# Optimization experiments

Hardware: AMD Instinct MI355X
Metric: run time of the kernel (lower is better)

Reference implementation:

```python
import math
import jax, jax.numpy as jnp
import numpy as np

HEAD_DIM = 128
NUM_HEADS = 16
NUM_KV_HEADS = 4
CAUSAL = True


def rotate_half(x):
    x1 = x[..., : x.shape[-1] // 2]
    x2 = x[..., x.shape[-1] // 2 :]
    return jnp.concatenate([-x2, x1], axis=-1)


def setup_inputs() -> dict:
    key = jax.random.key(0)
    k1, k2, k3, k4, k5 = jax.random.split(key, 5)
    B, S, H = 2, 2048, 2048
    total_heads = NUM_HEADS + 2 * NUM_KV_HEADS  # 24
    hidden_states = jax.random.normal(k1, (B, S, H), dtype=jnp.float32)
    cos = jax.random.normal(k2, (S, HEAD_DIM), dtype=jnp.float32)
    sin = jax.random.normal(k3, (S, HEAD_DIM), dtype=jnp.float32)
    # eqx.nn.Linear weight layout: [out_features, in_features], y = W @ x
    w_qkv = jax.random.normal(k4, (total_heads * HEAD_DIM, H), dtype=jnp.float32) / math.sqrt(H)
    w_o = jax.random.normal(k5, (H, NUM_HEADS * HEAD_DIM), dtype=jnp.float32) / math.sqrt(NUM_HEADS * HEAD_DIM)
    return {"hidden_states": hidden_states, "cos": cos, "sin": sin, "w_qkv": w_qkv, "w_o": w_o}


def reference(hidden_states, cos, sin, w_qkv, w_o):
    B, S, _ = hidden_states.shape
    # fused QKV projection: [B,S,total_heads,head_dim]
    qkv = jnp.einsum("bsh,oh->bso", hidden_states, w_qkv).reshape(B, S, -1, HEAD_DIM)
    q = qkv[:, :, :NUM_HEADS]
    k = qkv[:, :, NUM_HEADS : NUM_HEADS + NUM_KV_HEADS]
    v = qkv[:, :, NUM_HEADS + NUM_KV_HEADS :]
    # RoPE: cos/sin [S,head_dim] -> broadcast [S,1,head_dim] over heads
    c = cos[..., None, :]
    s_ = sin[..., None, :]
    q = q * c + rotate_half(q) * s_
    k = k * c + rotate_half(k) * s_
    # GQA: repeat K/V across query-head groups
    rep = NUM_HEADS // NUM_KV_HEADS
    k = jnp.repeat(k, rep, axis=2)
    v = jnp.repeat(v, rep, axis=2)
    scale = 1.0 / math.sqrt(HEAD_DIM)
    scores = jnp.einsum("bshd,bthd->bhst", q, k) * scale  # [B,H,S,S]
    if CAUSAL:
        mask = jnp.tril(jnp.ones((S, S), dtype=bool))[None, None]
        scores = jnp.where(mask, scores, jnp.float32(-1e10))
    attn = jax.nn.softmax(scores, axis=-1)
    out = jnp.einsum("bhst,bthd->bshd", attn, v).reshape(B, S, -1)
    return jnp.einsum("bsd,od->bso", out, w_o)
```

## Files before the change

### kernel.cpp

```cpp
#include <hip/hip_runtime.h>
#include <hip/hip_bf16.h>
#include <stdint.h>

typedef __hip_bfloat16 bf16;
typedef __attribute__((ext_vector_type(8))) __bf16 bf16x8;
typedef __attribute__((ext_vector_type(4))) float f32x4;
typedef __attribute__((ext_vector_type(16))) float f32x16;
typedef __attribute__((ext_vector_type(4))) unsigned int u32x4;

#define QSCALE_LOG2E (0.08838834764831845f * 1.4426950408889634f)

__device__ __forceinline__ float fast_exp2(float x) {
#if __has_builtin(__builtin_amdgcn_exp2f)
  return __builtin_amdgcn_exp2f(x);
#else
  return exp2f(x);
#endif
}

__device__ __forceinline__ void gload_lds16(const void* g, void* l) {
  __builtin_amdgcn_global_load_lds(
      (__attribute__((address_space(1))) void*)(uintptr_t)g,
      (__attribute__((address_space(3))) void*)(uint32_t)(uintptr_t)l,
      16, 0, 0);
}

__global__ void cast3(const float* __restrict__ h, const float* __restrict__ wq,
                      const float* __restrict__ wo, bf16* __restrict__ oh,
                      bf16* __restrict__ owq, bf16* __restrict__ owo) {
  const int total = 4718592;
  const int stride = gridDim.x * blockDim.x;
  for (int c = blockIdx.x * blockDim.x + threadIdx.x; c < total; c += stride) {
    const float* src;
    bf16* dst;
    int i;
    if (c < 2097152) { src = h; dst = oh; i = c; }
    else if (c < 3670016) { src = wq; dst = owq; i = c - 2097152; }
    else { src = wo; dst = owo; i = c - 3670016; }
    float4 v = reinterpret_cast<const float4*>(src)[i];
    bf16 tmp[4];
    tmp[0] = __float2bfloat16(v.x);
    tmp[1] = __float2bfloat16(v.y);
    tmp[2] = __float2bfloat16(v.z);
    tmp[3] = __float2bfloat16(v.w);
    reinterpret_cast<uint2*>(dst)[i] = *reinterpret_cast<uint2*>(tmp);
  }
}

__device__ __forceinline__ void store_c(float v, bf16* p) { *p = __float2bfloat16(v); }
__device__ __forceinline__ void store_c(float v, float* p) { *p = v; }

__device__ __forceinline__ bf16x8 rd_swz(const bf16* base, int row, int ks, int hi) {
  const int byte = row * 128 + ((ks * 64 + hi * 16) ^ ((row & 7) << 4));
  return *reinterpret_cast<const bf16x8*>((const char*)base + byte);
}

__device__ __forceinline__ void stage_part(const bf16* __restrict__ g, int K,
                                           int kt, bf16* ldsBase, int part,
                                           int tid) {
  const int ga = part * 512 + tid;
  const int r = ga >> 3;
  const int gl = ga & 7;
  const int col = kt * 64 + ((gl ^ (r & 7)) << 3);
  gload_lds16(g + (size_t)r * K + col, (char*)ldsBase + ga * 16);
}

#define DS_A(QR)                                                              \
  _Pragma("unroll") for (int m = 0; m < 4; ++m)                               \
  _Pragma("unroll") for (int ks = 0; ks < 2; ++ks)                            \
      af[m][ks] = rd_swz(Acur, wm * 128 + (QR) * 64 + m * 16 + lr, ks, hi);

#define DS_B0()                                                               \
  _Pragma("unroll") for (int n = 0; n < NQ0; ++n)                             \
  _Pragma("unroll") for (int ks = 0; ks < 2; ++ks)                            \
      bf0[n][ks] = rd_swz(Bcur, wn * WN + n * 16 + lr, ks, hi);

#define DS_B1()                                                               \
  _Pragma("unroll") for (int n = 0; n < NQ1; ++n)                             \
  _Pragma("unroll") for (int ks = 0; ks < 2; ++ks)                            \
      bf1[n][ks] = rd_swz(Bcur, wn * WN + (NQ0 + n) * 16 + lr, ks, hi);

#define MFMA_Q0(QR)                                                           \
  __builtin_amdgcn_s_setprio(1);                                             \
  _Pragma("unroll") for (int ks = 0; ks < 2; ++ks)                            \
  _Pragma("unroll") for (int m = 0; m < 4; ++m)                               \
  _Pragma("unroll") for (int n = 0; n < NQ0; ++n)                             \
      acc[(QR) * 4 + m][n] = __builtin_amdgcn_mfma_f32_16x16x32_bf16(         \
          af[m][ks], bf0[n][ks], acc[(QR) * 4 + m][n], 0, 0, 0);              \
  __builtin_amdgcn_s_setprio(0);

#define MFMA_Q1(QR)                                                           \
  __builtin_amdgcn_s_setprio(1);                                             \
  _Pragma("unroll") for (int ks = 0; ks < 2; ++ks)                            \
  _Pragma("unroll") for (int m = 0; m < 4; ++m)                               \
  _Pragma("unroll") for (int n = 0; n < NQ1; ++n)                             \
      acc[(QR) * 4 + m][NQ0 + n] = __builtin_amdgcn_mfma_f32_16x16x32_bf16(   \
          af[m][ks], bf1[n][ks], acc[(QR) * 4 + m][NQ0 + n], 0, 0, 0);        \
  __builtin_amdgcn_s_setprio(0);

#define PHASE_SYNC_PRE()                                \
  __builtin_amdgcn_s_barrier();                         \
  asm volatile("s_waitcnt lgkmcnt(0)" ::: "memory");    \
  __builtin_amdgcn_sched_barrier(0);

#define PHASE_END() __builtin_amdgcn_s_barrier();

#define VMCNT_LB()                                                            \
  if constexpr (LB == 2) asm volatile("s_waitcnt vmcnt(2)" ::: "memory");     \
  else if constexpr (LB == 3) asm volatile("s_waitcnt vmcnt(3)" ::: "memory");\
  else asm volatile("s_waitcnt vmcnt(4)" ::: "memory");

template <int BN, typename OutT>
__global__ __launch_bounds__(512, 2) void gemm256(const bf16* __restrict__ A,
                                                  const bf16* __restrict__ B,
                                                  OutT* __restrict__ C,
                                                  int M, int N, int K, int NBX) {
  constexpr int NFRAG = BN / 64;
  constexpr int NQ0 = (NFRAG + 1) / 2;
  constexpr int NQ1 = NFRAG - NQ0;
  constexpr int WN = BN / 4;
  constexpr int LB = BN / 64;
  constexpr int LB0 = (LB + 1) / 2;
  constexpr int LB1 = LB - LB0;

  extern __shared__ bf16 sm[];
  bf16* A0 = sm;
  bf16* A1 = sm + 16384;
  bf16* B0 = sm + 32768;
  bf16* B1 = B0 + BN * 64;

  const int tid = threadIdx.x;
  const int lane = tid & 63;
  const int w = tid >> 6;
  const int wm = w >> 2;
  const int wn = w & 3;
  const int lr = lane & 15;
  const int hi = lane >> 4;

  const int nwg = gridDim.x;
  const int cpx = nwg >> 3;
  const int bid = blockIdx.x;
  const int wg = (bid & 7) * cpx + (bid >> 3);
  const int bx = wg % NBX;
  const int by = wg / NBX;
  const int row0 = by * 256;
  const int col0 = bx * BN;

  const bf16* Ag = A + (size_t)row0 * K;
  const bf16* Bg = B + (size_t)col0 * K;

#pragma unroll
  for (int p = 0; p < 4; ++p) stage_part(Ag, K, 0, A0, p, tid);
#pragma unroll
  for (int p = 0; p < LB; ++p) stage_part(Bg, K, 0, B0, p, tid);
#pragma unroll
  for (int p = 0; p < LB; ++p) stage_part(Bg, K, 1, B1, p, tid);
  VMCNT_LB();
  __builtin_amdgcn_s_barrier();

  f32x4 acc[8][NFRAG] = {};
  bf16x8 af[4][2], bf0[NQ0][2], bf1[NQ1 ? NQ1 : 1][2];

  const int iters = K >> 7;
  for (int i = 0; i < iters; ++i) {
    const bool g2 = (i + 1 < iters);
    const int t1 = 2 * i + 1, t2 = 2 * i + 2, t3 = 2 * i + 3;
    {
      const bf16* Acur = A0;
      const bf16* Bcur = B0;
      DS_A(0); DS_B0();
      stage_part(Ag, K, t1, A1, 0, tid);
      stage_part(Ag, K, t1, A1, 1, tid);
      PHASE_SYNC_PRE(); MFMA_Q0(0); PHASE_END();
      DS_B1();
      stage_part(Ag, K, t1, A1, 2, tid);
      stage_part(Ag, K, t1, A1, 3, tid);
      PHASE_SYNC_PRE(); MFMA_Q1(0); PHASE_END();
      DS_A(1);
      if (g2) {
#pragma unroll
        for (int p = 0; p < LB0; ++p) stage_part(Bg, K, t2, B0, p, tid);
      }
      PHASE_SYNC_PRE(); MFMA_Q0(1); PHASE_END();
      if (g2) {
#pragma unroll
        for (int p = 0; p < LB1; ++p) stage_part(Bg, K, t2, B0, LB0 + p, tid);
        VMCNT_LB();
      } else {
        asm volatile("s_waitcnt vmcnt(0)" ::: "memory");
      }
      PHASE_SYNC_PRE(); MFMA_Q1(1); PHASE_END();
    }
    {
      const bf16* Acur = A1;
      const bf16* Bcur = B1;
      DS_A(0); DS_B0();
      if (g2) {
        stage_part(Ag, K, t2, A0, 0, tid);
        stage_part(Ag, K, t2, A0, 1, tid);
      }
      PHASE_SYNC_PRE(); MFMA_Q0(0); PHASE_END();
      DS_B1();
      if (g2) {
        stage_part(Ag, K, t2, A0, 2, tid);
        stage_part(Ag, K, t2, A0, 3, tid);
      }
      PHASE_SYNC_PRE(); MFMA_Q1(0); PHASE_END();
      DS_A(1);
      if (g2) {
#pragma unroll
        for (int p = 0; p < LB0; ++p) stage_part(Bg, K, t3, B1, p, tid);
      }
      PHASE_SYNC_PRE(); MFMA_Q0(1); PHASE_END();
      if (g2) {
#pragma unroll
        for (int p = 0; p < LB1; ++p) stage_part(Bg, K, t3, B1, LB0 + p, tid);
        VMCNT_LB();
      } else {
        asm volatile("s_waitcnt vmcnt(0)" ::: "memory");
      }
      PHASE_SYNC_PRE(); MFMA_Q1(1); PHASE_END();
    }
  }

#pragma unroll
  for (int mi = 0; mi < 8; ++mi)
#pragma unroll
    for (int ni = 0; ni < NFRAG; ++ni)
#pragma unroll
      for (int j = 0; j < 4; ++j) {
        const int r = row0 + wm * 128 + mi * 16 + hi * 4 + j;
        const int cc = col0 + wn * WN + ni * 16 + lr;
        store_c(acc[mi][ni][j], &C[(size_t)r * N + cc]);
      }
}

__global__ void rope_scatter(const bf16* __restrict__ qkv,
                             const float* __restrict__ cs,
                             const float* __restrict__ sn,
                             bf16* __restrict__ Q, bf16* __restrict__ Kd) {
  const int tok = blockIdx.x;
  const int b = tok >> 11;
  const int s = tok & 2047;
  const bf16* row = qkv + (size_t)tok * 3072;
  for (int idx = threadIdx.x; idx < 1280; idx += blockDim.x) {
    const int head = idx >> 6;
    const int j = idx & 63;
    float x1 = __bfloat162float(row[head * 128 + j]);
    float x2 = __bfloat162float(row[head * 128 + j + 64]);
    const float c1 = cs[s * 128 + j];
    const float c2 = cs[s * 128 + j + 64];
    const float s1 = sn[s * 128 + j];
    const float s2 = sn[s * 128 + j + 64];
    float y1 = x1 * c1 - x2 * s1;
    float y2 = x2 * c2 + x1 * s2;
    bf16* dst;
    if (head < 16) {
      y1 *= QSCALE_LOG2E;
      y2 *= QSCALE_LOG2E;
      dst = Q + ((size_t)(b * 16 + head) * 2048 + s) * 128;
    } else {
      dst = Kd + ((size_t)(b * 4 + head - 16) * 2048 + s) * 128;
    }
    dst[j] = __float2bfloat16(y1);
    dst[j + 64] = __float2bfloat16(y2);
  }
}

__global__ __launch_bounds__(256) void vtrans(const bf16* __restrict__ qkv,
                                              bf16* __restrict__ Vt) {
  __shared__ bf16 tile[64 * 136];
  const int bid = blockIdx.x;
  const int stile = bid & 31;
  const int hv = (bid >> 5) & 3;
  const int b = bid >> 7;
  const int tid = threadIdx.x;
  const int tok0 = stile * 64;
  const bf16* src = qkv + (size_t)(b * 2048 + tok0) * 3072 + 2560 + hv * 128;
#pragma unroll
  for (int i = 0; i < 4; ++i) {
    const int c = tid + i * 256;
    const int r = c >> 4;
    const int off = (c & 15) * 8;
    uint4 d = *reinterpret_cast<const uint4*>(src + (size_t)r * 3072 + off);
    *reinterpret_cast<uint4*>(&tile[r * 136 + off]) = d;
  }
  __syncthreads();
  bf16* dst = Vt + ((size_t)(b * 4 + hv) * 128) * 2048 + tok0;
#pragma unroll
  for (int i = 0; i < 4; ++i) {
    const int o = tid + i * 256;
    const int d = o >> 3;
    const int s0 = (o & 7) * 8;
    bf16 vals[8];
#pragma unroll
    for (int j = 0; j < 8; ++j) vals[j] = tile[(s0 + j) * 136 + d];
    *reinterpret_cast<uint4*>(dst + (size_t)d * 2048 + s0) =
        *reinterpret_cast<const uint4*>(vals);
  }
}

__device__ __forceinline__ void stage_k(const bf16* __restrict__ Kb, int k0,
                                        bf16* dst, int w, int lane) {
#pragma unroll
  for (int i = 0; i < 4; ++i) {
    const int L16 = i * 256 + w * 64 + lane;
    const int row = L16 >> 4;
    const int colb = (L16 & 15) * 16;
    const int src = colb ^ ((row & 7) << 4);
    gload_lds16(Kb + (size_t)(k0 + row) * 128 + (src >> 1),
                (char*)dst + (i * 256 + w * 64) * 16);
  }
}

__device__ __forceinline__ void stage_v(const bf16* __restrict__ Vtb, int k0,
                                        bf16* dst, int w, int lane) {
#pragma unroll
  for (int i = 0; i < 4; ++i) {
    const int L16 = i * 256 + w * 64 + lane;
    const int row = L16 >> 3;
    const int colb = (L16 & 7) * 16;
    const int src = colb ^ ((row & 7) << 4);
    gload_lds16(Vtb + (size_t)row * 2048 + k0 + (src >> 1),
                (char*)dst + (i * 256 + w * 64) * 16);
  }
}

__device__ __forceinline__ bf16x8 lds_read_swz(const bf16* base, int row,
                                               int colElem, int rowBytes) {
  const int byte = row * rowBytes + (((colElem * 2) ^ ((row & 7) << 4)));
  return *reinterpret_cast<const bf16x8*>((const char*)base + byte);
}

__global__ __launch_bounds__(256, 2) void attn_fwd(const bf16* __restrict__ Qg,
                                                   const bf16* __restrict__ Kg,
                                                   const bf16* __restrict__ Vtg,
                                                   bf16* __restrict__ Og) {
  __shared__ bf16 Ks[2][64 * 128];
  __shared__ bf16 Vs[2][128 * 64];

  const int tid = threadIdx.x;
  const int lane = tid & 63;
  const int w = tid >> 6;
  const int bid = blockIdx.x;
  int qt, bh;
  if (bid < 256) { qt = bid & 15; bh = bid >> 4; }
  else           { qt = 15 - (bid & 15); bh = 16 + ((bid - 256) >> 4); }
  const int b = bh >> 4;
  const int h = bh & 15;
  const int kvh = h >> 2;
  const int q31 = lane & 31;
  const int hw = lane >> 5;

  const bf16* Qb = Qg + ((size_t)(b * 16 + h) * 2048) * 128;
  const bf16* Kb = Kg + ((size_t)(b * 4 + kvh) * 2048) * 128;
  const bf16* Vtb = Vtg + ((size_t)(b * 4 + kvh) * 128) * 2048;

  const int qw = qt * 128 + w * 32;

  bf16x8 qf[8];
#pragma unroll
  for (int db = 0; db < 8; ++db)
    qf[db] = *reinterpret_cast<const bf16x8*>(Qb + (size_t)(qw + q31) * 128 +
                                              db * 16 + hw * 8);

  f32x16 acc[4] = {};
  float mrow = -1e30f;
  float lsum = 0.f;

  const int nt = 2 * qt + 2;

  stage_k(Kb, 0, &Ks[0][0], w, lane);
  stage_v(Vtb, 0, &Vs[0][0], w, lane);

  for (int t = 0; t < nt; ++t) {
    const int cur = t & 1;
    if (t + 1 < nt) {
      stage_k(Kb, (t + 1) * 64, &Ks[cur ^ 1][0], w, lane);
      stage_v(Vtb, (t + 1) * 64, &Vs[cur ^ 1][0], w, lane);
      asm volatile("s_waitcnt vmcnt(8)" ::: "memory");
    } else {
      asm volatile("s_waitcnt vmcnt(0)" ::: "memory");
    }
    __builtin_amdgcn_s_barrier();
    __builtin_amdgcn_sched_barrier(0);

    const int k0 = t * 64;
    const bool active = (k0 <= qw + 31);
    if (active) {
      const bf16* Kt = &Ks[cur][0];
      const bf16* Vtl = &Vs[cur][0];

      bf16x8 va[8];
#pragma unroll
      for (int i = 0; i < 8; ++i) {
        const int kb16 = i >> 2, db = i & 3;
        va[i] = lds_read_swz(Vtl, db * 32 + q31, kb16 * 16 + hw * 8, 128);
      }

      f32x16 sacc[2] = {};
      __builtin_amdgcn_s_setprio(1);
#pragma unroll
      for (int kb = 0; kb < 2; ++kb)
#pragma unroll
        for (int db = 0; db < 8; ++db) {
          bf16x8 kf = lds_read_swz(Kt, kb * 32 + q31, db * 16 + hw * 8, 256);
          sacc[kb] = __builtin_amdgcn_mfma_f32_32x32x16_bf16(kf, qf[db],
                                                             sacc[kb], 0, 0, 0);
        }
      __builtin_amdgcn_s_setprio(0);

      bf16x8 vb[8];
#pragma unroll
      for (int i = 0; i < 8; ++i) {
        const int kb16 = 2 + (i >> 2), db = i & 3;
        vb[i] = lds_read_swz(Vtl, db * 32 + q31, kb16 * 16 + hw * 8, 128);
      }

      float p[2][16];
#pragma unroll
      for (int kb = 0; kb < 2; ++kb)
#pragma unroll
        for (int r = 0; r < 16; ++r) p[kb][r] = sacc[kb][r];

      if (k0 + 63 > qw) {
        const int qg = qw + q31;
#pragma unroll
        for (int kb = 0; kb < 2; ++kb)
#pragma unroll
          for (int r = 0; r < 16; ++r) {
            const int k = k0 + kb * 32 + (r & 3) + 8 * (r >> 2) + 4 * hw;
            if (k > qg) p[kb][r] = -1e30f;
          }
      }

      float mt = p[0][0];
#pragma unroll
      for (int r = 1; r < 16; ++r) mt = fmaxf(mt, p[0][r]);
#pragma unroll
      for (int r = 0; r < 16; ++r) mt = fmaxf(mt, p[1][r]);
      mt = fmaxf(mt, __shfl_xor(mt, 32));

      if (__any(mt > mrow + 11.5f)) {
        const float mnew = fmaxf(mrow, mt);
        const float alpha = fast_exp2(mrow - mnew);
        mrow = mnew;
        lsum *= alpha;
        float areg[16];
#pragma unroll
        for (int r = 0; r < 16; ++r) {
          const int qloc = (r & 3) + 8 * (r >> 2) + 4 * hw;
          areg[r] = __shfl(alpha, qloc + (lane & 32));
        }
#pragma unroll
        for (int db = 0; db < 4; ++db)
#pragma unroll
          for (int r = 0; r < 16; ++r) acc[db][r] *= areg[r];
      }

      float rs = 0.f;
#pragma unroll
      for (int kb = 0; kb < 2; ++kb)
#pragma unroll
        for (int r = 0; r < 16; ++r) {
          const float pe = fast_exp2(p[kb][r] - mrow);
          p[kb][r] = pe;
          rs += pe;
        }
      rs += __shfl_xor(rs, 32);
      lsum += rs;

      unsigned int pk[2][8];
#pragma unroll
      for (int kb = 0; kb < 2; ++kb)
#pragma unroll
        for (int i = 0; i < 8; ++i)
          asm("v_cvt_pk_bf16_f32 %0, %1, %2"
              : "=v"(pk[kb][i])
              : "v"(p[kb][2 * i]), "v"(p[kb][2 * i + 1]));

#pragma unroll
      for (int kb16 = 0; kb16 < 4; ++kb16) {
        const int kb = kb16 >> 1;
        const int j0 = (kb16 & 1) * 4;
        unsigned int a0 = pk[kb][j0 + 0], b0 = pk[kb][j0 + 2];
        unsigned int a1 = pk[kb][j0 + 1], b1 = pk[kb][j0 + 3];
        asm volatile("v_permlane32_swap_b32 %0, %1" : "+v"(a0), "+v"(b0));
        asm volatile("v_permlane32_swap_b32 %0, %1" : "+v"(a1), "+v"(b1));
        u32x4 afu;
        afu.x = a0; afu.y = a1; afu.z = b0; afu.w = b1;
        bf16x8 pa;
        __builtin_memcpy(&pa, &afu, 16);
        __builtin_amdgcn_s_setprio(1);
#pragma unroll
        for (int db = 0; db < 4; ++db) {
          const bf16x8 vf = (kb16 < 2) ? va[kb16 * 4 + db] : vb[(kb16 - 2) * 4 + db];
          acc[db] = __builtin_amdgcn_mfma_f32_32x32x16_bf16(pa, vf,
                                                            acc[db], 0, 0, 0);
        }
        __builtin_amdgcn_s_setprio(0);
      }
    }

    __builtin_amdgcn_sched_barrier(0);
    __builtin_amdgcn_s_barrier();
  }

  const float inv = 1.0f / lsum;
  float invq[16];
#pragma unroll
  for (int r = 0; r < 16; ++r) {
    const int qloc = (r & 3) + 8 * (r >> 2) + 4 * hw;
    invq[r] = __shfl(inv, qloc + (lane & 32));
  }
#pragma unroll
  for (int db = 0; db < 4; ++db)
#pragma unroll
    for (int r = 0; r < 16; ++r) {
      const int qg = qw + (r & 3) + 8 * (r >> 2) + 4 * hw;
      const int dg = db * 32 + q31;
      Og[((size_t)(b * 2048 + qg)) * 2048 + h * 128 + dg] =
          __float2bfloat16(acc[db][r] * invq[r]);
    }
}

extern "C" void kernel_launch(void* const* d_in, const int* in_sizes, int n_in,
                              void* d_out, int out_size, void* d_ws,
                              size_t ws_size, hipStream_t stream) {
  const float* hidden = (const float*)d_in[0];
  const float* cs = (const float*)d_in[1];
  const float* sn = (const float*)d_in[2];
  const float* wqkv = (const float*)d_in[3];
  const float* wo = (const float*)d_in[4];
  float* out = (float*)d_out;

  bf16* p = (bf16*)d_ws;
  bf16* hid_b = p;   p += 8388608;
  bf16* wqkv_b = p;  p += 6291456;
  bf16* wo_b = p;    p += 4194304;
  bf16* qkv = p;     p += 12582912;
  bf16* Qs = p;      p += 8388608;
  bf16* Ksc = p;     p += 2097152;
  bf16* Vt = p;      p += 2097152;

  (void)hipFuncSetAttribute((const void*)gemm256<192, bf16>,
                            hipFuncAttributeMaxDynamicSharedMemorySize, 131072);
  (void)hipFuncSetAttribute((const void*)gemm256<128, float>,
                            hipFuncAttributeMaxDynamicSharedMemorySize, 131072);

  cast3<<<2048, 256, 0, stream>>>(hidden, wqkv, wo, hid_b, wqkv_b, wo_b);

  gemm256<192, bf16><<<256, 512, 114688, stream>>>(hid_b, wqkv_b, qkv,
                                                   4096, 3072, 2048, 16);
  rope_scatter<<<4096, 256, 0, stream>>>(qkv, cs, sn, Qs, Ksc);
  vtrans<<<256, 256, 0, stream>>>(qkv, Vt);

  bf16* aout = hid_b;
  attn_fwd<<<512, 256, 0, stream>>>(Qs, Ksc, Vt, aout);

  gemm256<128, float><<<256, 512, 98304, stream>>>(aout, wo_b, out,
                                                   4096, 2048, 2048, 16);
}
```

Before: 174.8 us.

## Give each attention wave two 32-row query tiles, halving block size

The attention kernel now runs 2 waves per block (128 threads) instead of 4, and each wave handles 64 query rows as two 32-row sub-tiles. Each K and V fragment read from LDS is reused across both sub-tiles, which halves LDS read traffic per MFMA. The staging loops are rewritten for 128 threads, with 8 loads each and a matching vmcnt wait. In exchange, per-wave register use roughly doubles (two accumulator sets, Q fragments and score tiles), and there are fewer waves per block to hide latency. The causal skip is also coarser, at 64-row granularity.

```diff
diff --git a/kernel.cpp b/kernel.cpp
--- a/kernel.cpp
+++ b/kernel.cpp
@@ -300,29 +300,29 @@
   }
 }
 
-__device__ __forceinline__ void stage_k(const bf16* __restrict__ Kb, int k0,
-                                        bf16* dst, int w, int lane) {
-#pragma unroll
-  for (int i = 0; i < 4; ++i) {
-    const int L16 = i * 256 + w * 64 + lane;
-    const int row = L16 >> 4;
-    const int colb = (L16 & 15) * 16;
+__device__ __forceinline__ void stage_k2(const bf16* __restrict__ Kb, int k0,
+                                         bf16* dst, int tid) {
+#pragma unroll
+  for (int i = 0; i < 8; ++i) {
+    const int ga = i * 128 + tid;
+    const int row = ga >> 4;
+    const int colb = (ga & 15) << 4;
     const int src = colb ^ ((row & 7) << 4);
     gload_lds16(Kb + (size_t)(k0 + row) * 128 + (src >> 1),
-                (char*)dst + (i * 256 + w * 64) * 16);
-  }
-}
-
-__device__ __forceinline__ void stage_v(const bf16* __restrict__ Vtb, int k0,
-                                        bf16* dst, int w, int lane) {
-#pragma unroll
-  for (int i = 0; i < 4; ++i) {
-    const int L16 = i * 256 + w * 64 + lane;
-    const int row = L16 >> 3;
-    const int colb = (L16 & 7) * 16;
+                (char*)dst + ga * 16);
+  }
+}
+
+__device__ __forceinline__ void stage_v2(const bf16* __restrict__ Vtb, int k0,
+                                         bf16* dst, int tid) {
+#pragma unroll
+  for (int i = 0; i < 8; ++i) {
+    const int ga = i * 128 + tid;
+    const int row = ga >> 3;
+    const int colb = (ga & 7) << 4;
     const int src = colb ^ ((row & 7) << 4);
     gload_lds16(Vtb + (size_t)row * 2048 + k0 + (src >> 1),
-                (char*)dst + (i * 256 + w * 64) * 16);
+                (char*)dst + ga * 16);
   }
 }
 
@@ -332,7 +332,7 @@
   return *reinterpret_cast<const bf16x8*>((const char*)base + byte);
 }
 
-__global__ __launch_bounds__(256, 2) void attn_fwd(const bf16* __restrict__ Qg,
+__global__ __launch_bounds__(128, 1) void attn_fwd(const bf16* __restrict__ Qg,
                                                    const bf16* __restrict__ Kg,
                                                    const bf16* __restrict__ Vtg,
                                                    bf16* __restrict__ Og) {
@@ -356,29 +356,31 @@
   const bf16* Kb = Kg + ((size_t)(b * 4 + kvh) * 2048) * 128;
   const bf16* Vtb = Vtg + ((size_t)(b * 4 + kvh) * 128) * 2048;
 
-  const int qw = qt * 128 + w * 32;
-
-  bf16x8 qf[8];
-#pragma unroll
-  for (int db = 0; db < 8; ++db)
-    qf[db] = *reinterpret_cast<const bf16x8*>(Qb + (size_t)(qw + q31) * 128 +
-                                              db * 16 + hw * 8);
-
-  f32x16 acc[4] = {};
-  float mrow = -1e30f;
-  float lsum = 0.f;
+  const int qw = qt * 128 + w * 64;
+
+  bf16x8 qf[2][8];
+#pragma unroll
+  for (int qt2 = 0; qt2 < 2; ++qt2)
+#pragma unroll
+    for (int db = 0; db < 8; ++db)
+      qf[qt2][db] = *reinterpret_cast<const bf16x8*>(
+          Qb + (size_t)(qw + qt2 * 32 + q31) * 128 + db * 16 + hw * 8);
+
+  f32x16 acc[2][4] = {};
+  float mrow[2] = {-1e30f, -1e30f};
+  float lsum[2] = {0.f, 0.f};
 
   const int nt = 2 * qt + 2;
 
-  stage_k(Kb, 0, &Ks[0][0], w, lane);
-  stage_v(Vtb, 0, &Vs[0][0], w, lane);
+  stage_k2(Kb, 0, &Ks[0][0], tid);
+  stage_v2(Vtb, 0, &Vs[0][0], tid);
 
   for (int t = 0; t < nt; ++t) {
     const int cur = t & 1;
     if (t + 1 < nt) {
-      stage_k(Kb, (t + 1) * 64, &Ks[cur ^ 1][0], w, lane);
-      stage_v(Vtb, (t + 1) * 64, &Vs[cur ^ 1][0], w, lane);
-      asm volatile("s_waitcnt vmcnt(8)" ::: "memory");
+      stage_k2(Kb, (t + 1) * 64, &Ks[cur ^ 1][0], tid);
+      stage_v2(Vtb, (t + 1) * 64, &Vs[cur ^ 1][0], tid);
+      asm volatile("s_waitcnt vmcnt(16)" ::: "memory");
     } else {
       asm volatile("s_waitcnt vmcnt(0)" ::: "memory");
     }
@@ -386,117 +388,126 @@
     __builtin_amdgcn_sched_barrier(0);
 
     const int k0 = t * 64;
-    const bool active = (k0 <= qw + 31);
-    if (active) {
+    if (k0 <= qw + 63) {
       const bf16* Kt = &Ks[cur][0];
       const bf16* Vtl = &Vs[cur][0];
 
-      bf16x8 va[8];
-#pragma unroll
-      for (int i = 0; i < 8; ++i) {
-        const int kb16 = i >> 2, db = i & 3;
-        va[i] = lds_read_swz(Vtl, db * 32 + q31, kb16 * 16 + hw * 8, 128);
-      }
-
-      f32x16 sacc[2] = {};
-      __builtin_amdgcn_s_setprio(1);
-#pragma unroll
-      for (int kb = 0; kb < 2; ++kb)
-#pragma unroll
-        for (int db = 0; db < 8; ++db) {
-          bf16x8 kf = lds_read_swz(Kt, kb * 32 + q31, db * 16 + hw * 8, 256);
-          sacc[kb] = __builtin_amdgcn_mfma_f32_32x32x16_bf16(kf, qf[db],
-                                                             sacc[kb], 0, 0, 0);
+      f32x16 sacc[2][2] = {};
+#pragma unroll
+      for (int kb = 0; kb < 2; ++kb) {
+        bf16x8 kf[8];
+#pragma unroll
+        for (int db = 0; db < 8; ++db)
+          kf[db] = lds_read_swz(Kt, kb * 32 + q31, db * 16 + hw * 8, 256);
+        __builtin_amdgcn_s_setprio(1);
+#pragma unroll
+        for (int qt2 = 0; qt2 < 2; ++qt2)
+#pragma unroll
+          for (int db = 0; db < 8; ++db)
+            sacc[qt2][kb] = __builtin_amdgcn_mfma_f32_32x32x16_bf16(
+                kf[db], qf[qt2][db], sacc[qt2][kb], 0, 0, 0);
+        __builtin_amdgcn_s_setprio(0);
+      }
+
+      float p[2][2][16];
+#pragma unroll
+      for (int qt2 = 0; qt2 < 2; ++qt2)
+#pragma unroll
+        for (int kb = 0; kb < 2; ++kb)
+#pragma unroll
+          for (int r = 0; r < 16; ++r) p[qt2][kb][r] = sacc[qt2][kb][r];
+
+#pragma unroll
+      for (int qt2 = 0; qt2 < 2; ++qt2) {
+        if (k0 + 63 > qw + qt2 * 32) {
+          const int qg = qw + qt2 * 32 + q31;
+#pragma unroll
+          for (int kb = 0; kb < 2; ++kb)
+#pragma unroll
+            for (int r = 0; r < 16; ++r) {
+              const int k = k0 + kb * 32 + (r & 3) + 8 * (r >> 2) + 4 * hw;
+              if (k > qg) p[qt2][kb][r] = -1e30f;
+            }
         }
-      __builtin_amdgcn_s_setprio(0);
-
-      bf16x8 vb[8];
-#pragma unroll
-      for (int i = 0; i < 8; ++i) {
-        const int kb16 = 2 + (i >> 2), db = i & 3;
-        vb[i] = lds_read_swz(Vtl, db * 32 + q31, kb16 * 16 + hw * 8, 128);
-      }
-
-      float p[2][16];
-#pragma unroll
-      for (int kb = 0; kb < 2; ++kb)
-#pragma unroll
-        for (int r = 0; r < 16; ++r) p[kb][r] = sacc[kb][r];
-
-      if (k0 + 63 > qw) {
-        const int qg = qw + q31;
+      }
+
+      float mt[2];
+#pragma unroll
+      for (int qt2 = 0; qt2 < 2; ++qt2) {
+        float m = p[qt2][0][0];
+#pragma unroll
+        for (int r = 1; r < 16; ++r) m = fmaxf(m, p[qt2][0][r]);
+#pragma unroll
+        for (int r = 0; r < 16; ++r) m = fmaxf(m, p[qt2][1][r]);
+        mt[qt2] = fmaxf(m, __shfl_xor(m, 32));
+      }
+
+      if (__any((mt[0] > mrow[0] + 11.5f) || (mt[1] > mrow[1] + 11.5f))) {
+#pragma unroll
+        for (int qt2 = 0; qt2 < 2; ++qt2) {
+          const float mnew = fmaxf(mrow[qt2], mt[qt2]);
+          const float alpha = fast_exp2(mrow[qt2] - mnew);
+          mrow[qt2] = mnew;
+          lsum[qt2] *= alpha;
+          float areg[16];
+#pragma unroll
+          for (int r = 0; r < 16; ++r) {
+            const int qloc = (r & 3) + 8 * (r >> 2) + 4 * hw;
+            areg[r] = __shfl(alpha, qloc + (lane & 32));
+          }
+#pragma unroll
+          for (int db = 0; db < 4; ++db)
+#pragma unroll
+            for (int r = 0; r < 16; ++r) acc[qt2][db][r] *= areg[r];
+        }
+      }
+
+      unsigned int pk[2][2][8];
+#pragma unroll
+      for (int qt2 = 0; qt2 < 2; ++qt2) {
+        float rs = 0.f;
 #pragma unroll
         for (int kb = 0; kb < 2; ++kb)
 #pragma unroll
           for (int r = 0; r < 16; ++r) {
-            const int k = k0 + kb * 32 + (r & 3) + 8 * (r >> 2) + 4 * hw;
-            if (k > qg) p[kb][r] = -1e30f;
+            const float pe = fast_exp2(p[qt2][kb][r] - mrow[qt2]);
+            p[qt2][kb][r] = pe;
+            rs += pe;
           }
-      }
-
-      float mt = p[0][0];
-#pragma unroll
-      for (int r = 1; r < 16; ++r) mt = fmaxf(mt, p[0][r]);
-#pragma unroll
-      for (int r = 0; r < 16; ++r) mt = fmaxf(mt, p[1][r]);
-      mt = fmaxf(mt, __shfl_xor(mt, 32));
-
-      if (__any(mt > mrow + 11.5f)) {
-        const float mnew = fmaxf(mrow, mt);
-        const float alpha = fast_exp2(mrow - mnew);
-        mrow = mnew;
-        lsum *= alpha;
-        float areg[16];
-#pragma unroll
-        for (int r = 0; r < 16; ++r) {
-          const int qloc = (r & 3) + 8 * (r >> 2) + 4 * hw;
-          areg[r] = __shfl(alpha, qloc + (lane & 32));
-        }
+        rs += __shfl_xor(rs, 32);
+        lsum[qt2] += rs;
+#pragma unroll
+        for (int kb = 0; kb < 2; ++kb)
+#pragma unroll
+          for (int i = 0; i < 8; ++i)
+            asm("v_cvt_pk_bf16_f32 %0, %1, %2"
+                : "=v"(pk[qt2][kb][i])
+                : "v"(p[qt2][kb][2 * i]), "v"(p[qt2][kb][2 * i + 1]));
+      }
+
+#pragma unroll
+      for (int kb16 = 0; kb16 < 4; ++kb16) {
+        bf16x8 vf[4];
 #pragma unroll
         for (int db = 0; db < 4; ++db)
-#pragma unroll
-          for (int r = 0; r < 16; ++r) acc[db][r] *= areg[r];
-      }
-
-      float rs = 0.f;
-#pragma unroll
-      for (int kb = 0; kb < 2; ++kb)
-#pragma unroll
-        for (int r = 0; r < 16; ++r) {
-          const float pe = fast_exp2(p[kb][r] - mrow);
-          p[kb][r] = pe;
-          rs += pe;
-        }
-      rs += __shfl_xor(rs, 32);
-      lsum += rs;
-
-      unsigned int pk[2][8];
-#pragma unroll
-      for (int kb = 0; kb < 2; ++kb)
-#pragma unroll
-        for (int i = 0; i < 8; ++i)
-          asm("v_cvt_pk_bf16_f32 %0, %1, %2"
-              : "=v"(pk[kb][i])
-              : "v"(p[kb][2 * i]), "v"(p[kb][2 * i + 1]));
-
-#pragma unroll
-      for (int kb16 = 0; kb16 < 4; ++kb16) {
-        const int kb = kb16 >> 1;
-        const int j0 = (kb16 & 1) * 4;
-        unsigned int a0 = pk[kb][j0 + 0], b0 = pk[kb][j0 + 2];
-        unsigned int a1 = pk[kb][j0 + 1], b1 = pk[kb][j0 + 3];
-        asm volatile("v_permlane32_swap_b32 %0, %1" : "+v"(a0), "+v"(b0));
-        asm volatile("v_permlane32_swap_b32 %0, %1" : "+v"(a1), "+v"(b1));
-        u32x4 afu;
-        afu.x = a0; afu.y = a1; afu.z = b0; afu.w = b1;
-        bf16x8 pa;
-        __builtin_memcpy(&pa, &afu, 16);
+          vf[db] = lds_read_swz(Vtl, db * 32 + q31, kb16 * 16 + hw * 8, 128);
         __builtin_amdgcn_s_setprio(1);
 #pragma unroll
-        for (int db = 0; db < 4; ++db) {
-          const bf16x8 vf = (kb16 < 2) ? va[kb16 * 4 + db] : vb[(kb16 - 2) * 4 + db];
-          acc[db] = __builtin_amdgcn_mfma_f32_32x32x16_bf16(pa, vf,
-                                                            acc[db], 0, 0, 0);
+        for (int qt2 = 0; qt2 < 2; ++qt2) {
+          const int kb = kb16 >> 1;
+          const int j0 = (kb16 & 1) * 4;
+          unsigned int a0 = pk[qt2][kb][j0 + 0], b0 = pk[qt2][kb][j0 + 2];
+          unsigned int a1 = pk[qt2][kb][j0 + 1], b1 = pk[qt2][kb][j0 + 3];
+          asm volatile("v_permlane32_swap_b32 %0, %1" : "+v"(a0), "+v"(b0));
+          asm volatile("v_permlane32_swap_b32 %0, %1" : "+v"(a1), "+v"(b1));
+          u32x4 afu;
+          afu.x = a0; afu.y = a1; afu.z = b0; afu.w = b1;
+          bf16x8 pa;
+          __builtin_memcpy(&pa, &afu, 16);
+#pragma unroll
+          for (int db = 0; db < 4; ++db)
+            acc[qt2][db] = __builtin_amdgcn_mfma_f32_32x32x16_bf16(
+                pa, vf[db], acc[qt2][db], 0, 0, 0);
         }
         __builtin_amdgcn_s_setprio(0);
       }
@@ -506,22 +517,25 @@
     __builtin_amdgcn_s_barrier();
   }
 
-  const float inv = 1.0f / lsum;
-  float invq[16];
-#pragma unroll
-  for (int r = 0; r < 16; ++r) {
-    const int qloc = (r & 3) + 8 * (r >> 2) + 4 * hw;
-    invq[r] = __shfl(inv, qloc + (lane & 32));
-  }
-#pragma unroll
-  for (int db = 0; db < 4; ++db)
+#pragma unroll
+  for (int qt2 = 0; qt2 < 2; ++qt2) {
+    const float inv = 1.0f / lsum[qt2];
+    float invq[16];
 #pragma unroll
     for (int r = 0; r < 16; ++r) {
-      const int qg = qw + (r & 3) + 8 * (r >> 2) + 4 * hw;
-      const int dg = db * 32 + q31;
-      Og[((size_t)(b * 2048 + qg)) * 2048 + h * 128 + dg] =
-          __float2bfloat16(acc[db][r] * invq[r]);
+      const int qloc = (r & 3) + 8 * (r >> 2) + 4 * hw;
+      invq[r] = __shfl(inv, qloc + (lane & 32));
     }
+#pragma unroll
+    for (int db = 0; db < 4; ++db)
+#pragma unroll
+      for (int r = 0; r < 16; ++r) {
+        const int qg = qw + qt2 * 32 + (r & 3) + 8 * (r >> 2) + 4 * hw;
+        const int dg = db * 32 + q31;
+        Og[((size_t)(b * 2048 + qg)) * 2048 + h * 128 + dg] =
+            __float2bfloat16(acc[qt2][db][r] * invq[r]);
+      }
+  }
 }
 
 extern "C" void kernel_launch(void* const* d_in, const int* in_sizes, int n_in,
@@ -556,7 +570,7 @@
   vtrans<<<256, 256, 0, stream>>>(qkv, Vt);
 
   bf16* aout = hid_b;
-  attn_fwd<<<512, 256, 0, stream>>>(Qs, Ksc, Vt, aout);
+  attn_fwd<<<512, 128, 0, stream>>>(Qs, Ksc, Vt, aout);
 
   gemm256<128, float><<<256, 512, 98304, stream>>>(aout, wo_b, out,
                                                    4096, 2048, 2048, 16);
```

Result: slower. 238.2 us (+36.3%).

## Triple-buffer A in GEMM with 64-wide K steps; load V fragments on demand

Applied to the files above, without the earlier changes.

The GEMM main loop changes from paired ping-pong steps over 128-wide K to a single 64-wide K-step loop. A gets three LDS buffers and is prefetched two tiles ahead, while B stays double-buffered and is prefetched one tile ahead. The goal is to hide more global-load latency, at the cost of more LDS per block (the dynamic shared size is raised to match). In attention, V fragments are now read from LDS right before each PV MFMA instead of being preloaded into registers, and the s_setprio hints are removed, which trades register pressure for LDS-read latency on the critical path.

```diff
diff --git a/kernel.cpp b/kernel.cpp
--- a/kernel.cpp
+++ b/kernel.cpp
@@ -105,11 +105,6 @@
 
 #define PHASE_END() __builtin_amdgcn_s_barrier();
 
-#define VMCNT_LB()                                                            \
-  if constexpr (LB == 2) asm volatile("s_waitcnt vmcnt(2)" ::: "memory");     \
-  else if constexpr (LB == 3) asm volatile("s_waitcnt vmcnt(3)" ::: "memory");\
-  else asm volatile("s_waitcnt vmcnt(4)" ::: "memory");
-
 template <int BN, typename OutT>
 __global__ __launch_bounds__(512, 2) void gemm256(const bf16* __restrict__ A,
                                                   const bf16* __restrict__ B,
@@ -120,14 +115,12 @@
   constexpr int NQ1 = NFRAG - NQ0;
   constexpr int WN = BN / 4;
   constexpr int LB = BN / 64;
-  constexpr int LB0 = (LB + 1) / 2;
-  constexpr int LB1 = LB - LB0;
+  constexpr int LB1 = (LB > 2) ? 2 : LB;
+  constexpr int LB2 = LB - LB1;
 
   extern __shared__ bf16 sm[];
-  bf16* A0 = sm;
-  bf16* A1 = sm + 16384;
-  bf16* B0 = sm + 32768;
-  bf16* B1 = B0 + BN * 64;
+  bf16* Ab = sm;
+  bf16* Bb = sm + 3 * 16384;
 
   const int tid = threadIdx.x;
   const int lane = tid & 63;
@@ -150,77 +143,52 @@
   const bf16* Bg = B + (size_t)col0 * K;
 
 #pragma unroll
-  for (int p = 0; p < 4; ++p) stage_part(Ag, K, 0, A0, p, tid);
-#pragma unroll
-  for (int p = 0; p < LB; ++p) stage_part(Bg, K, 0, B0, p, tid);
-#pragma unroll
-  for (int p = 0; p < LB; ++p) stage_part(Bg, K, 1, B1, p, tid);
-  VMCNT_LB();
+  for (int p = 0; p < 4; ++p) stage_part(Ag, K, 0, Ab, p, tid);
+#pragma unroll
+  for (int p = 0; p < 4; ++p) stage_part(Ag, K, 1, Ab + 16384, p, tid);
+#pragma unroll
+  for (int p = 0; p < LB; ++p) stage_part(Bg, K, 0, Bb, p, tid);
+  asm volatile("s_waitcnt vmcnt(0)" ::: "memory");
   __builtin_amdgcn_s_barrier();
 
   f32x4 acc[8][NFRAG] = {};
   bf16x8 af[4][2], bf0[NQ0][2], bf1[NQ1 ? NQ1 : 1][2];
 
-  const int iters = K >> 7;
-  for (int i = 0; i < iters; ++i) {
-    const bool g2 = (i + 1 < iters);
-    const int t1 = 2 * i + 1, t2 = 2 * i + 2, t3 = 2 * i + 3;
-    {
-      const bf16* Acur = A0;
-      const bf16* Bcur = B0;
-      DS_A(0); DS_B0();
-      stage_part(Ag, K, t1, A1, 0, tid);
-      stage_part(Ag, K, t1, A1, 1, tid);
-      PHASE_SYNC_PRE(); MFMA_Q0(0); PHASE_END();
-      DS_B1();
-      stage_part(Ag, K, t1, A1, 2, tid);
-      stage_part(Ag, K, t1, A1, 3, tid);
-      PHASE_SYNC_PRE(); MFMA_Q1(0); PHASE_END();
-      DS_A(1);
-      if (g2) {
-#pragma unroll
-        for (int p = 0; p < LB0; ++p) stage_part(Bg, K, t2, B0, p, tid);
-      }
-      PHASE_SYNC_PRE(); MFMA_Q0(1); PHASE_END();
-      if (g2) {
-#pragma unroll
-        for (int p = 0; p < LB1; ++p) stage_part(Bg, K, t2, B0, LB0 + p, tid);
-        VMCNT_LB();
-      } else {
-        asm volatile("s_waitcnt vmcnt(0)" ::: "memory");
-      }
-      PHASE_SYNC_PRE(); MFMA_Q1(1); PHASE_END();
-    }
-    {
-      const bf16* Acur = A1;
-      const bf16* Bcur = B1;
-      DS_A(0); DS_B0();
-      if (g2) {
-        stage_part(Ag, K, t2, A0, 0, tid);
-        stage_part(Ag, K, t2, A0, 1, tid);
-      }
-      PHASE_SYNC_PRE(); MFMA_Q0(0); PHASE_END();
-      DS_B1();
-      if (g2) {
-        stage_part(Ag, K, t2, A0, 2, tid);
-        stage_part(Ag, K, t2, A0, 3, tid);
-      }
-      PHASE_SYNC_PRE(); MFMA_Q1(0); PHASE_END();
-      DS_A(1);
-      if (g2) {
-#pragma unroll
-        for (int p = 0; p < LB0; ++p) stage_part(Bg, K, t3, B1, p, tid);
-      }
-      PHASE_SYNC_PRE(); MFMA_Q0(1); PHASE_END();
-      if (g2) {
-#pragma unroll
-        for (int p = 0; p < LB1; ++p) stage_part(Bg, K, t3, B1, LB0 + p, tid);
-        VMCNT_LB();
-      } else {
-        asm volatile("s_waitcnt vmcnt(0)" ::: "memory");
-      }
-      PHASE_SYNC_PRE(); MFMA_Q1(1); PHASE_END();
-    }
+  const int ntile = K >> 6;
+  for (int t = 0; t < ntile; ++t) {
+    const bf16* Acur = Ab + (t % 3) * 16384;
+    const bf16* Bcur = Bb + (t & 1) * (BN * 64);
+    bf16* Bnext = Bb + ((t + 1) & 1) * (BN * 64);
+    bf16* Anext2 = Ab + ((t + 2) % 3) * 16384;
+    const bool sB = (t + 1 < ntile);
+    const bool sA = (t + 2 < ntile);
+    DS_A(0); DS_B0();
+    if (sB) {
+#pragma unroll
+      for (int p = 0; p < LB1; ++p) stage_part(Bg, K, t + 1, Bnext, p, tid);
+    }
+    PHASE_SYNC_PRE(); MFMA_Q0(0); PHASE_END();
+    DS_B1();
+    if (sB && LB2 > 0) {
+#pragma unroll
+      for (int p = 0; p < LB2; ++p)
+        stage_part(Bg, K, t + 1, Bnext, LB1 + p, tid);
+    }
+    PHASE_SYNC_PRE(); MFMA_Q1(0); PHASE_END();
+    DS_A(1);
+    if (sA) {
+      stage_part(Ag, K, t + 2, Anext2, 0, tid);
+      stage_part(Ag, K, t + 2, Anext2, 1, tid);
+    }
+    PHASE_SYNC_PRE(); MFMA_Q0(1); PHASE_END();
+    if (sA) {
+      stage_part(Ag, K, t + 2, Anext2, 2, tid);
+      stage_part(Ag, K, t + 2, Anext2, 3, tid);
+      asm volatile("s_waitcnt vmcnt(4)" ::: "memory");
+    } else {
+      asm volatile("s_waitcnt vmcnt(0)" ::: "memory");
+    }
+    PHASE_SYNC_PRE(); MFMA_Q1(1); PHASE_END();
   }
 
 #pragma unroll
@@ -391,15 +359,7 @@
       const bf16* Kt = &Ks[cur][0];
       const bf16* Vtl = &Vs[cur][0];
 
-      bf16x8 va[8];
-#pragma unroll
-      for (int i = 0; i < 8; ++i) {
-        const int kb16 = i >> 2, db = i & 3;
-        va[i] = lds_read_swz(Vtl, db * 32 + q31, kb16 * 16 + hw * 8, 128);
-      }
-
       f32x16 sacc[2] = {};
-      __builtin_amdgcn_s_setprio(1);
 #pragma unroll
       for (int kb = 0; kb < 2; ++kb)
 #pragma unroll
@@ -408,14 +368,6 @@
           sacc[kb] = __builtin_amdgcn_mfma_f32_32x32x16_bf16(kf, qf[db],
                                                              sacc[kb], 0, 0, 0);
         }
-      __builtin_amdgcn_s_setprio(0);
-
-      bf16x8 vb[8];
-#pragma unroll
-      for (int i = 0; i < 8; ++i) {
-        const int kb16 = 2 + (i >> 2), db = i & 3;
-        vb[i] = lds_read_swz(Vtl, db * 32 + q31, kb16 * 16 + hw * 8, 128);
-      }
 
       float p[2][16];
 #pragma unroll
@@ -491,14 +443,12 @@
         afu.x = a0; afu.y = a1; afu.z = b0; afu.w = b1;
         bf16x8 pa;
         __builtin_memcpy(&pa, &afu, 16);
-        __builtin_amdgcn_s_setprio(1);
 #pragma unroll
         for (int db = 0; db < 4; ++db) {
-          const bf16x8 vf = (kb16 < 2) ? va[kb16 * 4 + db] : vb[(kb16 - 2) * 4 + db];
+          bf16x8 vf = lds_read_swz(Vtl, db * 32 + q31, kb16 * 16 + hw * 8, 128);
           acc[db] = __builtin_amdgcn_mfma_f32_32x32x16_bf16(pa, vf,
                                                             acc[db], 0, 0, 0);
         }
-        __builtin_amdgcn_s_setprio(0);
       }
     }
 
@@ -544,13 +494,13 @@
   bf16* Vt = p;      p += 2097152;
 
   (void)hipFuncSetAttribute((const void*)gemm256<192, bf16>,
-                            hipFuncAttributeMaxDynamicSharedMemorySize, 131072);
+                            hipFuncAttributeMaxDynamicSharedMemorySize, 147456);
   (void)hipFuncSetAttribute((const void*)gemm256<128, float>,
                             hipFuncAttributeMaxDynamicSharedMemorySize, 131072);
 
   cast3<<<2048, 256, 0, stream>>>(hidden, wqkv, wo, hid_b, wqkv_b, wo_b);
 
-  gemm256<192, bf16><<<256, 512, 114688, stream>>>(hid_b, wqkv_b, qkv,
+  gemm256<192, bf16><<<256, 512, 147456, stream>>>(hid_b, wqkv_b, qkv,
                                                    4096, 3072, 2048, 16);
   rope_scatter<<<4096, 256, 0, stream>>>(qkv, cs, sn, Qs, Ksc);
   vtrans<<<256, 256, 0, stream>>>(qkv, Vt);
@@ -558,6 +508,6 @@
   bf16* aout = hid_b;
   attn_fwd<<<512, 256, 0, stream>>>(Qs, Ksc, Vt, aout);
 
-  gemm256<128, float><<<256, 512, 98304, stream>>>(aout, wo_b, out,
-                                                   4096, 2048, 2048, 16);
-}
+  gemm256<128, float><<<256, 512, 131072, stream>>>(aout, wo_b, out,
+                                                    4096, 2048, 2048, 16);
+}
```

Result: slower. 178.4 us (+2.1%).
